# Kernel tuning notes

Hardware: AMD Instinct MI355X
Metric: run time of the kernel (lower is better)

The kernel has to match this reference:

```python
import jax, jax.numpy as jnp
import numpy as np

ALPHA = 0.15
CLIP = 5.0
EPS = 1e-6
LN_EPS = 1e-5

B, S, D, F = 4, 4096, 2048, 128


def setup_inputs() -> dict:
    key = jax.random.key(0)
    ks = jax.random.split(key, 8)
    sd = lambda fan_in: 1.0 / np.sqrt(fan_in)
    return {
        "x": jax.random.normal(ks[0], (B, S, D), dtype=jnp.float32),
        "Q_w": jax.random.normal(ks[1], (D, F), dtype=jnp.float32) * sd(D),
        "Q_b": jnp.zeros((F,), jnp.float32),
        "K_w": jax.random.normal(ks[2], (D, F), dtype=jnp.float32) * sd(D),
        "K_b": jnp.zeros((F,), jnp.float32),
        "lo_proj_w": jax.random.normal(ks[3], (D, D), dtype=jnp.float32) * sd(D),
        "lo_proj_b": jnp.zeros((D,), jnp.float32),
        "lo_p_w": jax.random.normal(ks[4], (D, F), dtype=jnp.float32) * sd(D),
        "lo_p_b": jnp.zeros((F,), jnp.float32),
        "proj_w": jax.random.normal(ks[5], (F, D), dtype=jnp.float32) * sd(F),
        "proj_b": jnp.zeros((D,), jnp.float32),
        "O_w": jax.random.normal(ks[6], (D // 2, D), dtype=jnp.float32) * sd(D // 2),
        "O_b": jnp.zeros((D,), jnp.float32),
        "ln_gamma": jnp.ones((D,), jnp.float32),
        "ln_beta": jnp.zeros((D,), jnp.float32),
    }


def _ema_over_time(score):
    # score: [B, S, F]; ema[0]=score[0]; ema[t]=a*score[t]+(1-a)*ema[t-1]
    seq = jnp.swapaxes(score, 0, 1)  # [S, B, F]

    def step(prev, x_t):
        new = ALPHA * x_t + (1.0 - ALPHA) * prev
        return new, new

    init = seq[0]
    _, rest = jax.lax.scan(step, init, seq[1:])
    ema_seq = jnp.concatenate([init[None], rest], axis=0)
    return jnp.swapaxes(ema_seq, 0, 1)


def reference(x, Q_w, Q_b, K_w, K_b, lo_proj_w, lo_proj_b, lo_p_w, lo_p_b,
              proj_w, proj_b, O_w, O_b, ln_gamma, ln_beta):
    x_f32 = x.astype(jnp.float32)
    residual = x_f32

    q = x_f32 @ Q_w + Q_b                    # [B,S,128]
    k = x_f32 @ K_w + K_b                    # [B,S,128]
    # Lo: Dense(d_model) -> gelu -> Dense(128)
    v_h = jax.nn.gelu(x_f32 @ lo_proj_w + lo_proj_b)
    V = v_h @ lo_p_w + lo_p_b                # [B,S,128]

    score = jax.nn.sigmoid(q) * jax.nn.sigmoid(k)
    score_ema = _ema_over_time(score)
    mean_last = jnp.mean(score_ema, axis=-1, keepdims=True)
    denom = jnp.maximum(mean_last, EPS)
    score_clipped = jnp.clip(score_ema / denom, -CLIP, CLIP)

    x_comb = score_clipped * V               # [B,S,128]
    out = x_comb @ proj_w + proj_b           # [B,S,D]  (D even -> no pad)
    a, b = jnp.split(out, 2, axis=-1)
    gated = jax.nn.silu(a) * b               # [B,S,D/2]
    out = gated @ O_w + O_b                  # [B,S,D]

    h = out + residual
    mu = jnp.mean(h, axis=-1, keepdims=True)
    var = jnp.var(h, axis=-1, keepdims=True)
    out = (h - mu) * jax.lax.rsqrt(var + LN_EPS) * ln_gamma + ln_beta
    return out.astype(x.dtype)
```

## Files before the change

### kernel.cpp

```cpp
#include <hip/hip_runtime.h>
#include <cstdint>

#define ALPHA_C 0.15f
#define ONE_MINUS_ALPHA 0.85f
#define CLIP_C 5.0f
#define EPS_C 1e-6f
#define LN_EPS_C 1e-5f

#define Bb 4
#define Ss 4096
#define Dd 2048
#define Mtot (Bb * Ss)

typedef __attribute__((ext_vector_type(8))) short bf16x8;
typedef __attribute__((ext_vector_type(4))) float f32x4;

__device__ __forceinline__ short f2bf(float f) {
  union { float f; uint32_t u; } v; v.f = f;
  uint32_t r = v.u + 0x7fffu + ((v.u >> 16) & 1u);
  return (short)(r >> 16);
}
__device__ __forceinline__ float bf2f(short s) {
  union { uint32_t u; float f; } v; v.u = ((uint32_t)(uint16_t)s) << 16;
  return v.f;
}
__device__ __forceinline__ float sigf(float x) { return 1.0f / (1.0f + __expf(-x)); }
__device__ __forceinline__ float geluf(float x) {
  const float c = 0.7978845608028654f;
  float x3 = x * x * x;
  return 0.5f * x * (1.0f + tanhf(c * (x + 0.044715f * x3)));
}

__device__ __forceinline__ void load_lds16(const short* g, short* l) {
  __builtin_amdgcn_global_load_lds((__attribute__((address_space(1))) void*)g,
                                   (__attribute__((address_space(3))) void*)l, 16, 0, 0);
}

#define BM 128
#define BN 128
#define BK 32

template <int MODE>
__global__ __launch_bounds__(256, 2) void gemm_tn(
    const short* __restrict__ A, const short* __restrict__ Bt, void* __restrict__ out0,
    void* __restrict__ out1, const float* __restrict__ bias, int M, int N, int K) {
  __shared__ __align__(16) short As[BM * BK];
  __shared__ __align__(16) short Bs[BN * BK];

  const int tid = threadIdx.x;
  const int wave = tid >> 6;
  const int lane = tid & 63;
  const int quad = lane >> 4;
  const int l16 = lane & 15;
  const int m0 = blockIdx.y * BM;
  const int n0 = blockIdx.x * BN;
  const int wm = (wave & 1) * 64;
  const int wn = (wave >> 1) * 64;

  const int srow = wave * 32 + (lane >> 2);
  const int skoff = ((lane & 3) ^ ((lane >> 3) & 3)) * 8;
  const short* agp = A + (long)(m0 + srow) * K + skoff;
  const short* bgp = Bt + (long)(n0 + srow) * K + skoff;
  const short* agp2 = agp + (long)16 * K;
  const short* bgp2 = bgp + (long)16 * K;
  short* al = As + (wave * 32) * BK;
  short* al2 = al + 16 * BK;
  short* bl = Bs + (wave * 32) * BK;
  short* bl2 = bl + 16 * BK;

  const int rsw = (l16 >> 1) & 3;

  f32x4 acc[4][4] = {};

  for (int k0 = 0; k0 < K; k0 += BK) {
    __syncthreads();
    load_lds16(agp + k0, al);
    load_lds16(agp2 + k0, al2);
    load_lds16(bgp + k0, bl);
    load_lds16(bgp2 + k0, bl2);
    __syncthreads();

    bf16x8 af[4], bfr[4];
#pragma unroll
    for (int i = 0; i < 4; ++i)
      af[i] = *(const bf16x8*)&As[(wm + i * 16 + l16) * BK + (quad ^ rsw) * 8];
#pragma unroll
    for (int j = 0; j < 4; ++j)
      bfr[j] = *(const bf16x8*)&Bs[(wn + j * 16 + l16) * BK + (quad ^ rsw) * 8];
#pragma unroll
    for (int i = 0; i < 4; ++i)
#pragma unroll
      for (int j = 0; j < 4; ++j)
        acc[i][j] = __builtin_amdgcn_mfma_f32_16x16x32_bf16(af[i], bfr[j], acc[i][j], 0, 0, 0);
  }

#pragma unroll
  for (int i = 0; i < 4; ++i) {
#pragma unroll
    for (int r = 0; r < 4; ++r) {
      const int row = m0 + wm + i * 16 + quad * 4 + r;
#pragma unroll
      for (int j = 0; j < 4; ++j) {
        const int col = n0 + wn + j * 16 + l16;
        float v = acc[i][j][r] + bias[col];
        if (MODE == 0) {
          ((float*)out0)[(long)row * N + col] = v;
        } else if (MODE == 1) {
          ((short*)out0)[(long)row * N + col] = f2bf(geluf(v));
        } else if (MODE == 2) {
          ((short*)out0)[(long)row * N + col] = f2bf(v);
        } else {
          if (n0 < 256)
            ((float*)out0)[(long)row * 256 + col] = v;
          else
            ((short*)out1)[(long)row * 2048 + (col - 256)] = f2bf(geluf(v));
        }
      }
    }
  }
}

__global__ __launch_bounds__(256) void cast_x_kernel(const float* __restrict__ in,
                                                     short* __restrict__ out, long n4) {
  long i = (long)blockIdx.x * blockDim.x + threadIdx.x;
  const long stride = (long)gridDim.x * blockDim.x;
  for (; i < n4; i += stride) {
    float4 v = ((const float4*)in)[i];
    short4 o;
    o.x = f2bf(v.x); o.y = f2bf(v.y); o.z = f2bf(v.z); o.w = f2bf(v.w);
    ((short4*)out)[i] = o;
  }
}

__global__ __launch_bounds__(256) void tcast_kernel(const float* __restrict__ in,
                                                    short* __restrict__ out, int R, int C) {
  __shared__ float t[32][33];
  const int c0 = blockIdx.x * 32, r0 = blockIdx.y * 32;
  const int tx = threadIdx.x, ty = threadIdx.y;
#pragma unroll
  for (int i = 0; i < 32; i += 8)
    t[ty + i][tx] = in[(long)(r0 + ty + i) * C + (c0 + tx)];
  __syncthreads();
#pragma unroll
  for (int i = 0; i < 32; i += 8)
    out[(long)(c0 + ty + i) * R + (r0 + tx)] = f2bf(t[tx][ty + i]);
}

__global__ void pack_bias_kernel(const float* __restrict__ qb, const float* __restrict__ kb,
                                 const float* __restrict__ lob, float* __restrict__ o) {
  int i = blockIdx.x * 256 + threadIdx.x;
  if (i < 128) o[i] = qb[i];
  else if (i < 256) o[i] = kb[i - 128];
  else if (i < 2304) o[i] = lob[i - 256];
}

#define SEG 64
#define WARM 96
__global__ __launch_bounds__(128) void ema_kernel(const float* __restrict__ qk,
                                                  float* __restrict__ ema) {
  const int f = threadIdx.x;
  const int b = blockIdx.y;
  const int seg = blockIdx.x;
  const int t0 = seg * SEG;
  const int tstart = (t0 >= WARM) ? (t0 - WARM) : 0;
  const int tend = t0 + SEG;
  const float* __restrict__ base = qk + (long)b * Ss * 256;
  float* __restrict__ eb = ema + (long)b * Ss * 128;

  float e;
  {
    float q = base[(long)tstart * 256 + f];
    float k = base[(long)tstart * 256 + 128 + f];
    e = sigf(q) * sigf(k);
  }
  if (seg == 0) eb[f] = e;

  int t = tstart + 1;
  const int CH = 8;
  const int nch = (tend - t) / CH;
  float cur[CH];
#pragma unroll
  for (int i = 0; i < CH; ++i) {
    float q = base[(long)(t + i) * 256 + f];
    float k = base[(long)(t + i) * 256 + 128 + f];
    cur[i] = ALPHA_C * (sigf(q) * sigf(k));
  }
  for (int c = 0; c < nch; ++c) {
    float nxt[CH] = {};
    if (c + 1 < nch) {
#pragma unroll
      for (int i = 0; i < CH; ++i) {
        float q = base[(long)(t + CH + i) * 256 + f];
        float k = base[(long)(t + CH + i) * 256 + 128 + f];
        nxt[i] = ALPHA_C * (sigf(q) * sigf(k));
      }
    }
#pragma unroll
    for (int i = 0; i < CH; ++i) {
      e = fmaf(ONE_MINUS_ALPHA, e, cur[i]);
      const int tt = t + i;
      if (tt >= t0) eb[(long)tt * 128 + f] = e;
    }
#pragma unroll
    for (int i = 0; i < CH; ++i) cur[i] = nxt[i];
    t += CH;
  }
  for (; t < tend; ++t) {
    float q = base[(long)t * 256 + f];
    float k = base[(long)t * 256 + 128 + f];
    e = fmaf(ONE_MINUS_ALPHA, e, ALPHA_C * (sigf(q) * sigf(k)));
    if (t >= t0) eb[(long)t * 128 + f] = e;
  }
}

__global__ __launch_bounds__(256) void comb_kernel(const float* __restrict__ ema,
                                                   const float* __restrict__ V,
                                                   short* __restrict__ xcomb) {
  const int wv = threadIdx.x >> 6;
  const int lane = threadIdx.x & 63;
  const long row = (long)blockIdx.x * 4 + wv;
  const float* er = ema + row * 128;
  float e0 = er[lane], e1 = er[lane + 64];
  float s = e0 + e1;
#pragma unroll
  for (int m = 1; m < 64; m <<= 1) s += __shfl_xor(s, m, 64);
  const float denom = fmaxf(s * (1.0f / 128.0f), EPS_C);
  const float inv = 1.0f / denom;
  const float c0 = fminf(fmaxf(e0 * inv, -CLIP_C), CLIP_C);
  const float c1 = fminf(fmaxf(e1 * inv, -CLIP_C), CLIP_C);
  const float* vr = V + row * 128;
  xcomb[row * 128 + lane] = f2bf(c0 * vr[lane]);
  xcomb[row * 128 + 64 + lane] = f2bf(c1 * vr[lane + 64]);
}

__global__ __launch_bounds__(256) void gate_kernel(const short* __restrict__ out4,
                                                   short* __restrict__ gated) {
  const long g = (long)blockIdx.x * 256 + threadIdx.x;
  const long r = g >> 8;
  const int i4 = (int)(g & 255) * 4;
  const short4 a4 = *(const short4*)&out4[r * 2048 + i4];
  const short4 b4 = *(const short4*)&out4[r * 2048 + 1024 + i4];
  float ax = bf2f(a4.x), ay = bf2f(a4.y), az = bf2f(a4.z), aw = bf2f(a4.w);
  short4 o;
  o.x = f2bf(ax * sigf(ax) * bf2f(b4.x));
  o.y = f2bf(ay * sigf(ay) * bf2f(b4.y));
  o.z = f2bf(az * sigf(az) * bf2f(b4.z));
  o.w = f2bf(aw * sigf(aw) * bf2f(b4.w));
  *(short4*)&gated[r * 1024 + i4] = o;
}

__global__ __launch_bounds__(256) void ln_kernel(float* __restrict__ io,
                                                 const float* __restrict__ x,
                                                 const float* __restrict__ gamma,
                                                 const float* __restrict__ beta) {
  const long row = blockIdx.x;
  const int tid = threadIdx.x;
  const int wv = tid >> 6, lane = tid & 63;
  float* rp = io + row * 2048;
  const float* xp = x + row * 2048;
  float4 v0 = ((const float4*)rp)[tid * 2];
  float4 v1 = ((const float4*)rp)[tid * 2 + 1];
  float4 x0 = ((const float4*)xp)[tid * 2];
  float4 x1 = ((const float4*)xp)[tid * 2 + 1];
  float h[8] = {v0.x + x0.x, v0.y + x0.y, v0.z + x0.z, v0.w + x0.w,
                v1.x + x1.x, v1.y + x1.y, v1.z + x1.z, v1.w + x1.w};
  float sum = 0.f, ss = 0.f;
#pragma unroll
  for (int i = 0; i < 8; ++i) { sum += h[i]; ss += h[i] * h[i]; }
#pragma unroll
  for (int m = 1; m < 64; m <<= 1) {
    sum += __shfl_xor(sum, m, 64);
    ss += __shfl_xor(ss, m, 64);
  }
  __shared__ float rs[4], rq[4];
  if (lane == 0) { rs[wv] = sum; rq[wv] = ss; }
  __syncthreads();
  sum = rs[0] + rs[1] + rs[2] + rs[3];
  ss = rq[0] + rq[1] + rq[2] + rq[3];
  const float mu = sum * (1.0f / 2048.0f);
  const float var = ss * (1.0f / 2048.0f) - mu * mu;
  const float rstd = rsqrtf(var + LN_EPS_C);
  const int c0 = tid * 8;
  float o[8];
#pragma unroll
  for (int i = 0; i < 8; ++i)
    o[i] = (h[i] - mu) * rstd * gamma[c0 + i] + beta[c0 + i];
  ((float4*)rp)[tid * 2]     = make_float4(o[0], o[1], o[2], o[3]);
  ((float4*)rp)[tid * 2 + 1] = make_float4(o[4], o[5], o[6], o[7]);
}

extern "C" void kernel_launch(void* const* d_in, const int* in_sizes, int n_in,
                              void* d_out, int out_size, void* d_ws, size_t ws_size,
                              hipStream_t stream) {
  const float* x         = (const float*)d_in[0];
  const float* Q_w       = (const float*)d_in[1];
  const float* Q_b       = (const float*)d_in[2];
  const float* K_w       = (const float*)d_in[3];
  const float* K_b       = (const float*)d_in[4];
  const float* lo_proj_w = (const float*)d_in[5];
  const float* lo_proj_b = (const float*)d_in[6];
  const float* lo_p_w    = (const float*)d_in[7];
  const float* lo_p_b    = (const float*)d_in[8];
  const float* proj_w    = (const float*)d_in[9];
  const float* proj_b    = (const float*)d_in[10];
  const float* O_w       = (const float*)d_in[11];
  const float* O_b       = (const float*)d_in[12];
  const float* ln_g      = (const float*)d_in[13];
  const float* ln_b      = (const float*)d_in[14];

  char* ws = (char*)d_ws;
  size_t off = 0;
  auto alloc = [&](size_t bytes) {
    char* p = ws + off;
    off += (bytes + 255) & ~(size_t)255;
    return p;
  };
  short* x16   = (short*)alloc((size_t)Mtot * Dd * 2);
  short* h16   = (short*)alloc((size_t)Mtot * Dd * 2);
  float* qk    = (float*)alloc((size_t)Mtot * 256 * 4);
  float* vbuf  = (float*)alloc((size_t)Mtot * 128 * 4);
  float* emab  = (float*)alloc((size_t)Mtot * 128 * 4);
  short* xcomb = (short*)alloc((size_t)Mtot * 128 * 2);
  short* gated = (short*)alloc((size_t)Mtot * 1024 * 2);
  short* wbig  = (short*)alloc((size_t)2304 * 2048 * 2);
  short* lpt   = (short*)alloc((size_t)128 * 2048 * 2);
  short* prjt  = (short*)alloc((size_t)2048 * 128 * 2);
  short* ot    = (short*)alloc((size_t)2048 * 1024 * 2);
  float* biasb = (float*)alloc(2304 * 4);
  float* outf  = (float*)d_out;
  short* out4b = (short*)d_out;

  cast_x_kernel<<<8192, 256, 0, stream>>>(x, x16, (long)Mtot * Dd / 4);
  tcast_kernel<<<dim3(4, 64), dim3(32, 8), 0, stream>>>(Q_w, wbig, 2048, 128);
  tcast_kernel<<<dim3(4, 64), dim3(32, 8), 0, stream>>>(K_w, wbig + 128 * 2048, 2048, 128);
  tcast_kernel<<<dim3(64, 64), dim3(32, 8), 0, stream>>>(lo_proj_w, wbig + 256 * 2048, 2048, 2048);
  tcast_kernel<<<dim3(4, 64), dim3(32, 8), 0, stream>>>(lo_p_w, lpt, 2048, 128);
  tcast_kernel<<<dim3(64, 4), dim3(32, 8), 0, stream>>>(proj_w, prjt, 128, 2048);
  tcast_kernel<<<dim3(64, 32), dim3(32, 8), 0, stream>>>(O_w, ot, 1024, 2048);
  pack_bias_kernel<<<9, 256, 0, stream>>>(Q_b, K_b, lo_proj_b, biasb);

  gemm_tn<3><<<dim3(18, 128), 256, 0, stream>>>(x16, wbig, qk, h16, biasb, Mtot, 2304, 2048);
  gemm_tn<0><<<dim3(1, 128), 256, 0, stream>>>(h16, lpt, vbuf, nullptr, lo_p_b, Mtot, 128, 2048);
  ema_kernel<<<dim3(Ss / SEG, 4), 128, 0, stream>>>(qk, emab);
  comb_kernel<<<Mtot / 4, 256, 0, stream>>>(emab, vbuf, xcomb);
  gemm_tn<2><<<dim3(16, 128), 256, 0, stream>>>(xcomb, prjt, out4b, nullptr, proj_b, Mtot, 2048, 128);
  gate_kernel<<<16384, 256, 0, stream>>>(out4b, gated);
  gemm_tn<0><<<dim3(16, 128), 256, 0, stream>>>(gated, ot, outf, nullptr, O_b, Mtot, 2048, 1024);
  ln_kernel<<<Mtot, 256, 0, stream>>>(outf, x, ln_g, ln_b);
}
```

Measured before the change: 749.4 us.

## Fuse sigmoid score and SiLU gate into GEMM epilogues, split-K the V GEMM

Q and K weight rows are interleaved so the first GEMM's epilogue can compute sigmoid(q)*sigmoid(k) with a lane shuffle and write a 128-wide score buffer. The proj GEMM likewise interleaves the a/b halves so its epilogue applies SiLU gating directly, which removes the separate gate kernel and the bf16 round trip of the full projection output. The narrow N=128 V GEMM becomes a 4-way split-K whose partials are summed in the comb kernel, reusing the x16 buffer as scratch. It also adds grouped block-index swizzling for L2 reuse and raises the launch-bounds occupancy hint from 2 to 4 blocks, which may add register pressure.

```diff
diff --git a/kernel.cpp b/kernel.cpp
--- a/kernel.cpp
+++ b/kernel.cpp
@@ -20,10 +20,6 @@
   uint32_t r = v.u + 0x7fffu + ((v.u >> 16) & 1u);
   return (short)(r >> 16);
 }
-__device__ __forceinline__ float bf2f(short s) {
-  union { uint32_t u; float f; } v; v.u = ((uint32_t)(uint16_t)s) << 16;
-  return v.f;
-}
 __device__ __forceinline__ float sigf(float x) { return 1.0f / (1.0f + __expf(-x)); }
 __device__ __forceinline__ float geluf(float x) {
   const float c = 0.7978845608028654f;
@@ -41,9 +37,10 @@
 #define BK 32
 
 template <int MODE>
-__global__ __launch_bounds__(256, 2) void gemm_tn(
+__global__ __launch_bounds__(256, 4) void gemm_tn(
     const short* __restrict__ A, const short* __restrict__ Bt, void* __restrict__ out0,
-    void* __restrict__ out1, const float* __restrict__ bias, int M, int N, int K) {
+    void* __restrict__ out1, const float* __restrict__ bias, int K, int lda, int ldb,
+    int ldc, int nbx, long pstride) {
   __shared__ __align__(16) short As[BM * BK];
   __shared__ __align__(16) short Bs[BN * BK];
 
@@ -52,17 +49,28 @@
   const int lane = tid & 63;
   const int quad = lane >> 4;
   const int l16 = lane & 15;
-  const int m0 = blockIdx.y * BM;
-  const int n0 = blockIdx.x * BN;
+
+  const int bid = blockIdx.x;
+  const int panel = bid / (8 * nbx);
+  const int rem = bid - panel * (8 * nbx);
+  const int by = panel * 8 + (rem & 7);
+  const int bx = rem >> 3;
+  const int m0 = by * BM;
+  const int n0 = bx * BN;
   const int wm = (wave & 1) * 64;
   const int wn = (wave >> 1) * 64;
 
+  if (MODE == 5) {
+    A += (long)blockIdx.y * K;
+    Bt += (long)blockIdx.y * K;
+  }
+
   const int srow = wave * 32 + (lane >> 2);
   const int skoff = ((lane & 3) ^ ((lane >> 3) & 3)) * 8;
-  const short* agp = A + (long)(m0 + srow) * K + skoff;
-  const short* bgp = Bt + (long)(n0 + srow) * K + skoff;
-  const short* agp2 = agp + (long)16 * K;
-  const short* bgp2 = bgp + (long)16 * K;
+  const short* agp = A + (long)(m0 + srow) * lda + skoff;
+  const short* bgp = Bt + (long)(n0 + srow) * ldb + skoff;
+  const short* agp2 = agp + (long)16 * lda;
+  const short* bgp2 = bgp + (long)16 * ldb;
   short* al = As + (wave * 32) * BK;
   short* al2 = al + 16 * BK;
   short* bl = Bs + (wave * 32) * BK;
@@ -102,18 +110,25 @@
 #pragma unroll
       for (int j = 0; j < 4; ++j) {
         const int col = n0 + wn + j * 16 + l16;
-        float v = acc[i][j][r] + bias[col];
+        float v = acc[i][j][r];
+        if (MODE != 5) v += bias[col];
         if (MODE == 0) {
-          ((float*)out0)[(long)row * N + col] = v;
-        } else if (MODE == 1) {
-          ((short*)out0)[(long)row * N + col] = f2bf(geluf(v));
-        } else if (MODE == 2) {
-          ((short*)out0)[(long)row * N + col] = f2bf(v);
-        } else {
-          if (n0 < 256)
-            ((float*)out0)[(long)row * 256 + col] = v;
-          else
+          ((float*)out0)[(long)row * ldc + col] = v;
+        } else if (MODE == 5) {
+          float* o = (float*)out0 + (long)blockIdx.y * pstride;
+          o[(long)row * ldc + col] = v;
+        } else if (MODE == 3) {
+          if (n0 < 256) {
+            float sh = __shfl_xor(v, 1);
+            if (!(lane & 1))
+              ((float*)out0)[(long)row * 128 + (col >> 1)] = sigf(v) * sigf(sh);
+          } else {
             ((short*)out1)[(long)row * 2048 + (col - 256)] = f2bf(geluf(v));
+          }
+        } else if (MODE == 4) {
+          float sh = __shfl_xor(v, 1);
+          if (!(lane & 1))
+            ((short*)out0)[(long)row * 1024 + (col >> 1)] = f2bf(v * sigf(v) * sh);
         }
       }
     }
@@ -132,6 +147,7 @@
   }
 }
 
+template <int MAP>
 __global__ __launch_bounds__(256) void tcast_kernel(const float* __restrict__ in,
                                                     short* __restrict__ out, int R, int C) {
   __shared__ float t[32][33];
@@ -142,21 +158,30 @@
     t[ty + i][tx] = in[(long)(r0 + ty + i) * C + (c0 + tx)];
   __syncthreads();
 #pragma unroll
-  for (int i = 0; i < 32; i += 8)
-    out[(long)(c0 + ty + i) * R + (r0 + tx)] = f2bf(t[tx][ty + i]);
+  for (int i = 0; i < 32; i += 8) {
+    const int c = c0 + ty + i;
+    const int orow = (MAP == 0) ? c
+                   : (MAP == 1) ? 2 * c
+                   : (MAP == 2) ? 2 * c + 1
+                                : (c < 1024 ? 2 * c : 2 * (c - 1024) + 1);
+    out[(long)orow * R + (r0 + tx)] = f2bf(t[tx][ty + i]);
+  }
 }
 
 __global__ void pack_bias_kernel(const float* __restrict__ qb, const float* __restrict__ kb,
                                  const float* __restrict__ lob, float* __restrict__ o) {
   int i = blockIdx.x * 256 + threadIdx.x;
-  if (i < 128) o[i] = qb[i];
-  else if (i < 256) o[i] = kb[i - 128];
+  if (i < 256) o[i] = (i & 1) ? kb[i >> 1] : qb[i >> 1];
   else if (i < 2304) o[i] = lob[i - 256];
+}
+__global__ void pack_pbias_kernel(const float* __restrict__ pjb, float* __restrict__ o) {
+  int i = blockIdx.x * 256 + threadIdx.x;
+  o[i] = (i & 1) ? pjb[1024 + (i >> 1)] : pjb[i >> 1];
 }
 
 #define SEG 64
 #define WARM 96
-__global__ __launch_bounds__(128) void ema_kernel(const float* __restrict__ qk,
+__global__ __launch_bounds__(128) void ema_kernel(const float* __restrict__ score,
                                                   float* __restrict__ ema) {
   const int f = threadIdx.x;
   const int b = blockIdx.y;
@@ -164,15 +189,10 @@
   const int t0 = seg * SEG;
   const int tstart = (t0 >= WARM) ? (t0 - WARM) : 0;
   const int tend = t0 + SEG;
-  const float* __restrict__ base = qk + (long)b * Ss * 256;
+  const float* __restrict__ base = score + (long)b * Ss * 128;
   float* __restrict__ eb = ema + (long)b * Ss * 128;
 
-  float e;
-  {
-    float q = base[(long)tstart * 256 + f];
-    float k = base[(long)tstart * 256 + 128 + f];
-    e = sigf(q) * sigf(k);
-  }
+  float e = base[(long)tstart * 128 + f];
   if (seg == 0) eb[f] = e;
 
   int t = tstart + 1;
@@ -180,20 +200,12 @@
   const int nch = (tend - t) / CH;
   float cur[CH];
 #pragma unroll
-  for (int i = 0; i < CH; ++i) {
-    float q = base[(long)(t + i) * 256 + f];
-    float k = base[(long)(t + i) * 256 + 128 + f];
-    cur[i] = ALPHA_C * (sigf(q) * sigf(k));
-  }
+  for (int i = 0; i < CH; ++i) cur[i] = ALPHA_C * base[(long)(t + i) * 128 + f];
   for (int c = 0; c < nch; ++c) {
     float nxt[CH] = {};
     if (c + 1 < nch) {
 #pragma unroll
-      for (int i = 0; i < CH; ++i) {
-        float q = base[(long)(t + CH + i) * 256 + f];
-        float k = base[(long)(t + CH + i) * 256 + 128 + f];
-        nxt[i] = ALPHA_C * (sigf(q) * sigf(k));
-      }
+      for (int i = 0; i < CH; ++i) nxt[i] = ALPHA_C * base[(long)(t + CH + i) * 128 + f];
     }
 #pragma unroll
     for (int i = 0; i < CH; ++i) {
@@ -206,15 +218,14 @@
     t += CH;
   }
   for (; t < tend; ++t) {
-    float q = base[(long)t * 256 + f];
-    float k = base[(long)t * 256 + 128 + f];
-    e = fmaf(ONE_MINUS_ALPHA, e, ALPHA_C * (sigf(q) * sigf(k)));
+    e = fmaf(ONE_MINUS_ALPHA, e, ALPHA_C * base[(long)t * 128 + f]);
     if (t >= t0) eb[(long)t * 128 + f] = e;
   }
 }
 
 __global__ __launch_bounds__(256) void comb_kernel(const float* __restrict__ ema,
-                                                   const float* __restrict__ V,
+                                                   const float* __restrict__ vpart,
+                                                   const float* __restrict__ lob,
                                                    short* __restrict__ xcomb) {
   const int wv = threadIdx.x >> 6;
   const int lane = threadIdx.x & 63;
@@ -228,25 +239,15 @@
   const float inv = 1.0f / denom;
   const float c0 = fminf(fmaxf(e0 * inv, -CLIP_C), CLIP_C);
   const float c1 = fminf(fmaxf(e1 * inv, -CLIP_C), CLIP_C);
-  const float* vr = V + row * 128;
-  xcomb[row * 128 + lane] = f2bf(c0 * vr[lane]);
-  xcomb[row * 128 + 64 + lane] = f2bf(c1 * vr[lane + 64]);
-}
-
-__global__ __launch_bounds__(256) void gate_kernel(const short* __restrict__ out4,
-                                                   short* __restrict__ gated) {
-  const long g = (long)blockIdx.x * 256 + threadIdx.x;
-  const long r = g >> 8;
-  const int i4 = (int)(g & 255) * 4;
-  const short4 a4 = *(const short4*)&out4[r * 2048 + i4];
-  const short4 b4 = *(const short4*)&out4[r * 2048 + 1024 + i4];
-  float ax = bf2f(a4.x), ay = bf2f(a4.y), az = bf2f(a4.z), aw = bf2f(a4.w);
-  short4 o;
-  o.x = f2bf(ax * sigf(ax) * bf2f(b4.x));
-  o.y = f2bf(ay * sigf(ay) * bf2f(b4.y));
-  o.z = f2bf(az * sigf(az) * bf2f(b4.z));
-  o.w = f2bf(aw * sigf(aw) * bf2f(b4.w));
-  *(short4*)&gated[r * 1024 + i4] = o;
+  const long PS = (long)Mtot * 128;
+  float va = lob[lane], vb = lob[lane + 64];
+#pragma unroll
+  for (int p = 0; p < 4; ++p) {
+    va += vpart[p * PS + row * 128 + lane];
+    vb += vpart[p * PS + row * 128 + lane + 64];
+  }
+  xcomb[row * 128 + lane] = f2bf(c0 * va);
+  xcomb[row * 128 + 64 + lane] = f2bf(c1 * vb);
 }
 
 __global__ __launch_bounds__(256) void ln_kernel(float* __restrict__ io,
@@ -317,8 +318,7 @@
   };
   short* x16   = (short*)alloc((size_t)Mtot * Dd * 2);
   short* h16   = (short*)alloc((size_t)Mtot * Dd * 2);
-  float* qk    = (float*)alloc((size_t)Mtot * 256 * 4);
-  float* vbuf  = (float*)alloc((size_t)Mtot * 128 * 4);
+  float* score = (float*)alloc((size_t)Mtot * 128 * 4);
   float* emab  = (float*)alloc((size_t)Mtot * 128 * 4);
   short* xcomb = (short*)alloc((size_t)Mtot * 128 * 2);
   short* gated = (short*)alloc((size_t)Mtot * 1024 * 2);
@@ -327,24 +327,29 @@
   short* prjt  = (short*)alloc((size_t)2048 * 128 * 2);
   short* ot    = (short*)alloc((size_t)2048 * 1024 * 2);
   float* biasb = (float*)alloc(2304 * 4);
+  float* pbias = (float*)alloc(2048 * 4);
+  float* vpart = (float*)x16;
   float* outf  = (float*)d_out;
-  short* out4b = (short*)d_out;
 
   cast_x_kernel<<<8192, 256, 0, stream>>>(x, x16, (long)Mtot * Dd / 4);
-  tcast_kernel<<<dim3(4, 64), dim3(32, 8), 0, stream>>>(Q_w, wbig, 2048, 128);
-  tcast_kernel<<<dim3(4, 64), dim3(32, 8), 0, stream>>>(K_w, wbig + 128 * 2048, 2048, 128);
-  tcast_kernel<<<dim3(64, 64), dim3(32, 8), 0, stream>>>(lo_proj_w, wbig + 256 * 2048, 2048, 2048);
-  tcast_kernel<<<dim3(4, 64), dim3(32, 8), 0, stream>>>(lo_p_w, lpt, 2048, 128);
-  tcast_kernel<<<dim3(64, 4), dim3(32, 8), 0, stream>>>(proj_w, prjt, 128, 2048);
-  tcast_kernel<<<dim3(64, 32), dim3(32, 8), 0, stream>>>(O_w, ot, 1024, 2048);
+  tcast_kernel<1><<<dim3(4, 64), dim3(32, 8), 0, stream>>>(Q_w, wbig, 2048, 128);
+  tcast_kernel<2><<<dim3(4, 64), dim3(32, 8), 0, stream>>>(K_w, wbig, 2048, 128);
+  tcast_kernel<0><<<dim3(64, 64), dim3(32, 8), 0, stream>>>(lo_proj_w, wbig + 256 * 2048, 2048, 2048);
+  tcast_kernel<0><<<dim3(4, 64), dim3(32, 8), 0, stream>>>(lo_p_w, lpt, 2048, 128);
+  tcast_kernel<3><<<dim3(64, 4), dim3(32, 8), 0, stream>>>(proj_w, prjt, 128, 2048);
+  tcast_kernel<0><<<dim3(64, 32), dim3(32, 8), 0, stream>>>(O_w, ot, 1024, 2048);
   pack_bias_kernel<<<9, 256, 0, stream>>>(Q_b, K_b, lo_proj_b, biasb);
-
-  gemm_tn<3><<<dim3(18, 128), 256, 0, stream>>>(x16, wbig, qk, h16, biasb, Mtot, 2304, 2048);
-  gemm_tn<0><<<dim3(1, 128), 256, 0, stream>>>(h16, lpt, vbuf, nullptr, lo_p_b, Mtot, 128, 2048);
-  ema_kernel<<<dim3(Ss / SEG, 4), 128, 0, stream>>>(qk, emab);
-  comb_kernel<<<Mtot / 4, 256, 0, stream>>>(emab, vbuf, xcomb);
-  gemm_tn<2><<<dim3(16, 128), 256, 0, stream>>>(xcomb, prjt, out4b, nullptr, proj_b, Mtot, 2048, 128);
-  gate_kernel<<<16384, 256, 0, stream>>>(out4b, gated);
-  gemm_tn<0><<<dim3(16, 128), 256, 0, stream>>>(gated, ot, outf, nullptr, O_b, Mtot, 2048, 1024);
+  pack_pbias_kernel<<<8, 256, 0, stream>>>(proj_b, pbias);
+
+  gemm_tn<3><<<18 * 128, 256, 0, stream>>>(x16, wbig, score, h16, biasb,
+                                           2048, 2048, 2048, 0, 18, 0);
+  ema_kernel<<<dim3(Ss / SEG, 4), 128, 0, stream>>>(score, emab);
+  gemm_tn<5><<<dim3(128, 4), 256, 0, stream>>>(h16, lpt, vpart, nullptr, nullptr,
+                                               512, 2048, 2048, 128, 1, (long)Mtot * 128);
+  comb_kernel<<<Mtot / 4, 256, 0, stream>>>(emab, vpart, lo_p_b, xcomb);
+  gemm_tn<4><<<16 * 128, 256, 0, stream>>>(xcomb, prjt, gated, nullptr, pbias,
+                                           128, 128, 128, 1024, 16, 0);
+  gemm_tn<0><<<16 * 128, 256, 0, stream>>>(gated, ot, outf, nullptr, O_b,
+                                           1024, 1024, 1024, 2048, 16, 0);
   ln_kernel<<<Mtot, 256, 0, stream>>>(outf, x, ln_g, ln_b);
 }
```

Result: faster. 728.7 us (-2.8%).
